# Performance work log

Hardware: AMD Instinct MI355X
Metric: run time of the kernel (lower is better)

## Reference

```python
import jax, jax.numpy as jnp
import numpy as np

B, T, E, H = 4, 1024, 1024, 16
F = E // H  # head_feature = 64
EPS = 1e-5


def setup_inputs() -> dict:
    key = jax.random.key(0)
    ks = jax.random.split(key, 7)
    return {
        "x": jax.random.normal(ks[0], (B, T, E), dtype=jnp.float32),
        "q_w": jax.random.normal(ks[1], (H, E, F), dtype=jnp.float32),
        "k_w": jax.random.normal(ks[2], (H, E, F), dtype=jnp.float32),
        "v_w": jax.random.normal(ks[3], (H, E, F), dtype=jnp.float32),
        "fr_w": jax.random.normal(ks[4], (B, E, E), dtype=jnp.float32),
        "ff_w": jax.random.normal(ks[5], (E, E), dtype=jnp.float32),
        "ff_b": jax.random.normal(ks[6], (E,), dtype=jnp.float32),
        "ln1_w": jnp.ones((T, E), dtype=jnp.float32),
        "ln1_b": jnp.zeros((T, E), dtype=jnp.float32),
        "ln2_w": jnp.ones((T, E), dtype=jnp.float32),
        "ln2_b": jnp.zeros((T, E), dtype=jnp.float32),
    }


def _layernorm_2d(x, w, b):
    # LayerNorm over the last TWO dims ([T, E]), matching nn.LayerNorm([T, E])
    mean = jnp.mean(x, axis=(-2, -1), keepdims=True)
    var = jnp.mean(jnp.square(x - mean), axis=(-2, -1), keepdims=True)
    return (x - mean) * jax.lax.rsqrt(var + EPS) * w + b


def _attention(x, q_w, k_w, v_w, fr_w):
    # projections: [B,T,E] x [H,E,F] -> [B,H,T,F]
    q = jnp.einsum("bte,hef->bhtf", x, q_w)
    k = jnp.einsum("bte,hef->bhtf", x, k_w)
    v = jnp.einsum("bte,hef->bhtf", x, v_w)
    scores = jnp.einsum("bhqf,bhkf->bhqk", q, k)  # [B,H,T,T]
    # faithful to source: multiplicative mask (-1e9 on strict upper tri, +1 added everywhere)
    ones = jnp.ones((T, T), dtype=scores.dtype)
    mask = -1.0e9 * jnp.triu(ones, k=1) + ones
    scores = scores * mask
    attn = jax.nn.softmax(scores / jnp.sqrt(jnp.float32(F)), axis=-1)
    z = jnp.einsum("bhqk,bhkf->bhqf", attn, v)  # [B,H,T,F]
    z = z.transpose(0, 2, 1, 3).reshape(B, T, E)  # merge heads
    return jnp.einsum("bte,bed->btd", z, fr_w)  # per-batch feature reduction


def reference(x, q_w, k_w, v_w, fr_w, ff_w, ff_b, ln1_w, ln1_b, ln2_w, ln2_b):
    z = _attention(x, q_w, k_w, v_w, fr_w)
    z1 = _layernorm_2d(x + z, ln1_w, ln1_b)
    z2 = jax.nn.relu(jnp.einsum("bte,de->btd", z1, ff_w) + ff_b)
    return _layernorm_2d(z1 + z2, ln2_w, ln2_b)
```

## Files before the change

kernel.cpp:

```cpp
#include <hip/hip_runtime.h>
#include <math.h>

constexpr int Bc = 4, Tc = 1024, Ec = 1024, Hc = 16, Fc = 64;

typedef __attribute__((ext_vector_type(8))) short bf16x8;
typedef __attribute__((ext_vector_type(4))) float f32x4;

__device__ __forceinline__ ushort f2bf(float x) {
  union { float f; unsigned u; } v; v.f = x;
  unsigned r = v.u + 0x7fffu + ((v.u >> 16) & 1u);
  return (ushort)(r >> 16);
}
__device__ __forceinline__ float bf2f(ushort h) {
  union { float f; unsigned u; } v; v.u = ((unsigned)h) << 16; return v.f;
}
__device__ __forceinline__ void split3(float x, ushort& h, ushort& m, ushort& l) {
  h = f2bf(x);
  float r1 = x - bf2f(h);
  m = f2bf(r1);
  float r2 = r1 - bf2f(m);
  l = f2bf(r2);
}
__device__ __forceinline__ void split2(float x, ushort& h, ushort& l) {
  h = f2bf(x);
  l = f2bf(x - bf2f(h));
}
__device__ __forceinline__ void split3t(float x, ushort& h, ushort& m, ushort& l) {
  union { float f; unsigned u; } v; v.f = x;
  h = (ushort)(v.u >> 16);
  union { float f; unsigned u; } hf; hf.u = v.u & 0xffff0000u;
  float r1 = x - hf.f;
  union { float f; unsigned u; } v1; v1.f = r1;
  m = (ushort)(v1.u >> 16);
  union { float f; unsigned u; } mf; mf.u = v1.u & 0xffff0000u;
  float r2 = r1 - mf.f;
  union { float f; unsigned u; } v2; v2.f = r2;
  l = (ushort)(v2.u >> 16);
}

#define FRAG_IDX(tile, quad, l) (((((tile) * 4) + (quad)) * 16 + (l)) * 8)

__global__ __launch_bounds__(256) void prep_all(
    const float* __restrict__ qw, const float* __restrict__ kw,
    const float* __restrict__ vw, ushort* __restrict__ wT,
    const float* __restrict__ x, ushort* __restrict__ xh,
    ushort* __restrict__ xm, ushort* __restrict__ xl)
{
  const int zi = blockIdx.z;
  const int tid = threadIdx.x;
  if (zi >= 3) {
    const int bid = (zi - 3) * 256 + blockIdx.y * 16 + blockIdx.x;
    const int i = bid * 256 + tid;
    const float4 a = ((const float4*)x)[i * 2];
    const float4 b = ((const float4*)x)[i * 2 + 1];
    const float xs[8] = {a.x, a.y, a.z, a.w, b.x, b.y, b.z, b.w};
    bf16x8 h, m, l;
#pragma unroll
    for (int j = 0; j < 8; ++j) {
      ushort hu, mu, lu;
      split3t(xs[j], hu, mu, lu);
      h[j] = (short)hu; m[j] = (short)mu; l[j] = (short)lu;
    }
    ((bf16x8*)xh)[i] = h;
    ((bf16x8*)xm)[i] = m;
    ((bf16x8*)xl)[i] = l;
    return;
  }
  const float* src = (zi == 0) ? qw : (zi == 1) ? kw : vw;
  ushort* dst = wT + (size_t)(zi * 3) * (1u << 20);
  const int ns = (zi == 2) ? 1 : 3;
  const int h = blockIdx.y, e0 = blockIdx.x * 64;
  __shared__ float T[64][68];
  {
    const int er = tid >> 4, fr = (tid & 15) * 4;
#pragma unroll
    for (int i = 0; i < 4; ++i) {
      const float4 v = *(const float4*)&src[((size_t)(h * 1024 + e0 + er + i * 16)) * 64 + fr];
      *(float4*)&T[er + i * 16][fr] = v;
    }
  }
  __syncthreads();
  const int f = tid >> 2, eo = (tid & 3) * 16;
  ushort hs[16], ms[16], ls[16];
#pragma unroll
  for (int j = 0; j < 16; ++j) split3(T[eo + j][f], hs[j], ms[j], ls[j]);
  const size_t nbase = (size_t)(h * 64 + f) * 1024 + e0 + eo;
  bf16x8 v0, v1;
#pragma unroll
  for (int j = 0; j < 8; ++j) { v0[j] = (short)hs[j]; v1[j] = (short)hs[j + 8]; }
  *(bf16x8*)&dst[nbase] = v0; *(bf16x8*)&dst[nbase + 8] = v1;
  if (ns == 3) {
#pragma unroll
    for (int j = 0; j < 8; ++j) { v0[j] = (short)ms[j]; v1[j] = (short)ms[j + 8]; }
    *(bf16x8*)&dst[(1u << 20) + nbase] = v0; *(bf16x8*)&dst[(1u << 20) + nbase + 8] = v1;
#pragma unroll
    for (int j = 0; j < 8; ++j) { v0[j] = (short)ls[j]; v1[j] = (short)ls[j + 8]; }
    *(bf16x8*)&dst[(2u << 20) + nbase] = v0; *(bf16x8*)&dst[(2u << 20) + nbase + 8] = v1;
  }
}

__global__ __launch_bounds__(256) void transp_frw(
    const float* __restrict__ frw, ushort* __restrict__ frT)
{
  const int bb = blockIdx.z;
  const int e0 = blockIdx.x * 64, d0 = blockIdx.y * 64;
  __shared__ float T[64][68];
  const int tid = threadIdx.x;
  {
    const int er = tid >> 4, dr = (tid & 15) * 4;
#pragma unroll
    for (int i = 0; i < 4; ++i) {
      const float4 v = *(const float4*)&frw[((size_t)bb * 1024 + e0 + er + i * 16) * 1024 + d0 + dr];
      *(float4*)&T[er + i * 16][dr] = v;
    }
  }
  __syncthreads();
  const int d = tid >> 2, eo = (tid & 3) * 16;
  ushort hs[16], ls[16];
#pragma unroll
  for (int j = 0; j < 16; ++j) split2(T[eo + j][d], hs[j], ls[j]);
  const size_t nbase = ((size_t)bb * 1024 + d0 + d) * 1024 + e0 + eo;
  bf16x8 v0, v1;
#pragma unroll
  for (int j = 0; j < 8; ++j) { v0[j] = (short)hs[j]; v1[j] = (short)hs[j + 8]; }
  *(bf16x8*)&frT[nbase] = v0; *(bf16x8*)&frT[nbase + 8] = v1;
#pragma unroll
  for (int j = 0; j < 8; ++j) { v0[j] = (short)ls[j]; v1[j] = (short)ls[j + 8]; }
  *(bf16x8*)&frT[(4u << 20) + nbase] = v0; *(bf16x8*)&frT[(4u << 20) + nbase + 8] = v1;
}

__global__ __launch_bounds__(256) void proj_all_ps(
    const ushort* __restrict__ xh, const ushort* __restrict__ xm,
    const ushort* __restrict__ xl, const ushort* __restrict__ wT,
    float* __restrict__ qf, ushort* __restrict__ kh,
    ushort* __restrict__ km, ushort* __restrict__ kl,
    ushort* __restrict__ vt)
{
  const int zi = blockIdx.z;
  const int m0 = blockIdx.x * 128, n0 = blockIdx.y * 128;
  __shared__ ushort As[3 * 4096];
  __shared__ ushort Bs[3 * 4096];
  const int tid = threadIdx.x;
  const int wave = tid >> 6, lane = tid & 63, l15 = lane & 15, quad = lane >> 4;
  const int wm = wave >> 1, wn = wave & 1;
  const int sr = tid >> 1, q0 = (tid & 1) * 2;
  const int wb0 = FRAG_IDX(sr >> 4, q0, sr & 15);
  const int wb1 = FRAG_IDX(sr >> 4, q0 + 1, sr & 15);
  f32x4 acc[4][4] = {};

  const size_t arow = (size_t)(m0 + sr) * 1024 + q0 * 8;
  const ushort* axh = xh + arow;
  const ushort* axm = xm + arow;
  const ushort* axl = xl + arow;

  if (zi < 2) {
    const ushort* wt = wT + (size_t)zi * 3 * (1u << 20);
    const ushort* bpb = wt + (size_t)(n0 + sr) * 1024 + q0 * 8;
    bf16x8 pah0 = *(const bf16x8*)(axh);
    bf16x8 pah1 = *(const bf16x8*)(axh + 8);
    bf16x8 pam0 = *(const bf16x8*)(axm);
    bf16x8 pam1 = *(const bf16x8*)(axm + 8);
    bf16x8 pal0 = *(const bf16x8*)(axl);
    bf16x8 pal1 = *(const bf16x8*)(axl + 8);
    bf16x8 pb0[3], pb1[3];
#pragma unroll
    for (int s = 0; s < 3; ++s) {
      const ushort* bp = bpb + ((size_t)s << 20);
      pb0[s] = *(const bf16x8*)(bp);
      pb1[s] = *(const bf16x8*)(bp + 8);
    }
    for (int k0 = 0; k0 < 1024; k0 += 32) {
      __syncthreads();
      {
        *(bf16x8*)&As[wb0] = pah0;        *(bf16x8*)&As[wb1] = pah1;
        *(bf16x8*)&As[4096 + wb0] = pam0; *(bf16x8*)&As[4096 + wb1] = pam1;
        *(bf16x8*)&As[8192 + wb0] = pal0; *(bf16x8*)&As[8192 + wb1] = pal1;
#pragma unroll
        for (int s = 0; s < 3; ++s) {
          *(bf16x8*)&Bs[s * 4096 + wb0] = pb0[s];
          *(bf16x8*)&Bs[s * 4096 + wb1] = pb1[s];
        }
      }
      __syncthreads();
      if (k0 < 992) {
        const int ko = k0 + 32;
        pah0 = *(const bf16x8*)(axh + ko);
        pah1 = *(const bf16x8*)(axh + ko + 8);
        pam0 = *(const bf16x8*)(axm + ko);
        pam1 = *(const bf16x8*)(axm + ko + 8);
        pal0 = *(const bf16x8*)(axl + ko);
        pal1 = *(const bf16x8*)(axl + ko + 8);
#pragma unroll
        for (int s = 0; s < 3; ++s) {
          const ushort* bp = bpb + ((size_t)s << 20) + ko;
          pb0[s] = *(const bf16x8*)(bp);
          pb1[s] = *(const bf16x8*)(bp + 8);
        }
      }
      bf16x8 af[4][3];
#pragma unroll
      for (int tm = 0; tm < 4; ++tm)
#pragma unroll
        for (int s = 0; s < 3; ++s)
          af[tm][s] = *(const bf16x8*)&As[s * 4096 + FRAG_IDX(wm * 4 + tm, quad, l15)];
#pragma unroll
      for (int tn = 0; tn < 4; ++tn) {
        const int bi = FRAG_IDX(wn * 4 + tn, quad, l15);
        bf16x8 b0 = *(const bf16x8*)&Bs[bi];
        bf16x8 b1 = *(const bf16x8*)&Bs[4096 + bi];
        bf16x8 b2 = *(const bf16x8*)&Bs[8192 + bi];
#pragma unroll
        for (int tm = 0; tm < 4; ++tm) {
          f32x4 a = acc[tm][tn];
          a = __builtin_amdgcn_mfma_f32_16x16x32_bf16(af[tm][0], b0, a, 0, 0, 0);
          a = __builtin_amdgcn_mfma_f32_16x16x32_bf16(af[tm][0], b1, a, 0, 0, 0);
          a = __builtin_amdgcn_mfma_f32_16x16x32_bf16(af[tm][1], b0, a, 0, 0, 0);
          a = __builtin_amdgcn_mfma_f32_16x16x32_bf16(af[tm][0], b2, a, 0, 0, 0);
          a = __builtin_amdgcn_mfma_f32_16x16x32_bf16(af[tm][1], b1, a, 0, 0, 0);
          a = __builtin_amdgcn_mfma_f32_16x16x32_bf16(af[tm][2], b0, a, 0, 0, 0);
          acc[tm][tn] = a;
        }
      }
    }
#pragma unroll
    for (int tm = 0; tm < 4; ++tm) {
#pragma unroll
      for (int tn = 0; tn < 4; ++tn) {
#pragma unroll
        for (int r = 0; r < 4; ++r) {
          int m = m0 + wm * 64 + tm * 16 + quad * 4 + r;
          int n = n0 + wn * 64 + tn * 16 + l15;
          int b = m >> 10, t = m & 1023, h = n >> 6, f = n & 63;
          size_t idx = (((size_t)(b * 16 + h)) * 1024 + t) * 64 + f;
          if (zi == 0) {
            qf[idx] = acc[tm][tn][r];
          } else {
            ushort hu, mu, lu;
            split3(acc[tm][tn][r], hu, mu, lu);
            kh[idx] = hu; km[idx] = mu; kl[idx] = lu;
          }
        }
      }
    }
  } else {
    const ushort* wt = wT + (size_t)6 * (1u << 20);
    const ushort* bpb = wt + (size_t)(n0 + sr) * 1024 + q0 * 8;
    bf16x8 pah0 = *(const bf16x8*)(axh);
    bf16x8 pah1 = *(const bf16x8*)(axh + 8);
    bf16x8 pb0 = *(const bf16x8*)(bpb);
    bf16x8 pb1 = *(const bf16x8*)(bpb + 8);
    for (int k0 = 0; k0 < 1024; k0 += 32) {
      __syncthreads();
      {
        *(bf16x8*)&As[wb0] = pah0; *(bf16x8*)&As[wb1] = pah1;
        *(bf16x8*)&Bs[wb0] = pb0;  *(bf16x8*)&Bs[wb1] = pb1;
      }
      __syncthreads();
      if (k0 < 992) {
        const int ko = k0 + 32;
        pah0 = *(const bf16x8*)(axh + ko);
        pah1 = *(const bf16x8*)(axh + ko + 8);
        pb0 = *(const bf16x8*)(bpb + ko);
        pb1 = *(const bf16x8*)(bpb + ko + 8);
      }
      bf16x8 af[4];
#pragma unroll
      for (int tm = 0; tm < 4; ++tm)
        af[tm] = *(const bf16x8*)&As[FRAG_IDX(wm * 4 + tm, quad, l15)];
#pragma unroll
      for (int tn = 0; tn < 4; ++tn) {
        bf16x8 b0 = *(const bf16x8*)&Bs[FRAG_IDX(wn * 4 + tn, quad, l15)];
#pragma unroll
        for (int tm = 0; tm < 4; ++tm)
          acc[tm][tn] = __builtin_amdgcn_mfma_f32_16x16x32_bf16(af[tm], b0, acc[tm][tn], 0, 0, 0);
      }
    }
#pragma unroll
    for (int tm = 0; tm < 4; ++tm) {
#pragma unroll
      for (int tn = 0; tn < 4; ++tn) {
#pragma unroll
        for (int r = 0; r < 4; ++r) {
          int m = m0 + wm * 64 + tm * 16 + quad * 4 + r;
          int n = n0 + wn * 64 + tn * 16 + l15;
          int b = m >> 10, t = m & 1023, h = n >> 6, f = n & 63;
          vt[(((size_t)(b * 16 + h)) * 64 + f) * 1024 + t] = f2bf(acc[tm][tn][r]);
        }
      }
    }
  }
}

__global__ __launch_bounds__(256) void proj_all_mfma(
    const float* __restrict__ x, const ushort* __restrict__ wT,
    float* __restrict__ qf, ushort* __restrict__ kh,
    ushort* __restrict__ km, ushort* __restrict__ kl,
    ushort* __restrict__ vt)
{
  const int zi = blockIdx.z;
  const int m0 = blockIdx.x * 128, n0 = blockIdx.y * 128;
  __shared__ ushort As[3 * 4096];
  __shared__ ushort Bs[3 * 4096];
  const int tid = threadIdx.x;
  const int wave = tid >> 6, lane = tid & 63, l15 = lane & 15, quad = lane >> 4;
  const int wm = wave >> 1, wn = wave & 1;
  const int sr = tid >> 1, q0 = (tid & 1) * 2;
  const int wb0 = FRAG_IDX(sr >> 4, q0, sr & 15);
  const int wb1 = FRAG_IDX(sr >> 4, q0 + 1, sr & 15);
  f32x4 acc[4][4] = {};

  const float* apx = x + (size_t)(m0 + sr) * 1024 + q0 * 8;
  float4 px0 = *(const float4*)(apx);
  float4 px1 = *(const float4*)(apx + 4);
  float4 px2 = *(const float4*)(apx + 8);
  float4 px3 = *(const float4*)(apx + 12);

  if (zi < 2) {
    const ushort* wt = wT + (size_t)zi * 3 * (1u << 20);
    const ushort* bpb = wt + (size_t)(n0 + sr) * 1024 + q0 * 8;
    bf16x8 pb0[3], pb1[3];
#pragma unroll
    for (int s = 0; s < 3; ++s) {
      const ushort* bp = bpb + ((size_t)s << 20);
      pb0[s] = *(const bf16x8*)(bp);
      pb1[s] = *(const bf16x8*)(bp + 8);
    }
    for (int k0 = 0; k0 < 1024; k0 += 32) {
      __syncthreads();
      {
        float xs[16];
        *(float4*)&xs[0]  = px0;
        *(float4*)&xs[4]  = px1;
        *(float4*)&xs[8]  = px2;
        *(float4*)&xs[12] = px3;
        bf16x8 h0, h1, m0v, m1v, l0, l1;
#pragma unroll
        for (int j = 0; j < 8; ++j) {
          ushort hu, mu, lu;
          split3t(xs[j], hu, mu, lu);
          h0[j] = (short)hu; m0v[j] = (short)mu; l0[j] = (short)lu;
          split3t(xs[j + 8], hu, mu, lu);
          h1[j] = (short)hu; m1v[j] = (short)mu; l1[j] = (short)lu;
        }
        *(bf16x8*)&As[wb0] = h0;          *(bf16x8*)&As[wb1] = h1;
        *(bf16x8*)&As[4096 + wb0] = m0v;  *(bf16x8*)&As[4096 + wb1] = m1v;
        *(bf16x8*)&As[8192 + wb0] = l0;   *(bf16x8*)&As[8192 + wb1] = l1;
#pragma unroll
        for (int s = 0; s < 3; ++s) {
          *(bf16x8*)&Bs[s * 4096 + wb0] = pb0[s];
          *(bf16x8*)&Bs[s * 4096 + wb1] = pb1[s];
        }
      }
      __syncthreads();
      if (k0 < 992) {
        const float* nx = apx + k0 + 32;
        px0 = *(const float4*)(nx);
        px1 = *(const float4*)(nx + 4);
        px2 = *(const float4*)(nx + 8);
        px3 = *(const float4*)(nx + 12);
#pragma unroll
        for (int s = 0; s < 3; ++s) {
          const ushort* bp = bpb + ((size_t)s << 20) + k0 + 32;
          pb0[s] = *(const bf16x8*)(bp);
          pb1[s] = *(const bf16x8*)(bp + 8);
        }
      }
      bf16x8 af[4][3];
#pragma unroll
      for (int tm = 0; tm < 4; ++tm)
#pragma unroll
        for (int s = 0; s < 3; ++s)
          af[tm][s] = *(const bf16x8*)&As[s * 4096 + FRAG_IDX(wm * 4 + tm, quad, l15)];
#pragma unroll
      for (int tn = 0; tn < 4; ++tn) {
        const int bi = FRAG_IDX(wn * 4 + tn, quad, l15);
        bf16x8 b0 = *(const bf16x8*)&Bs[bi];
        bf16x8 b1 = *(const bf16x8*)&Bs[4096 + bi];
        bf16x8 b2 = *(const bf16x8*)&Bs[8192 + bi];
#pragma unroll
        for (int tm = 0; tm < 4; ++tm) {
          f32x4 a = acc[tm][tn];
          a = __builtin_amdgcn_mfma_f32_16x16x32_bf16(af[tm][0], b0, a, 0, 0, 0);
          a = __builtin_amdgcn_mfma_f32_16x16x32_bf16(af[tm][0], b1, a, 0, 0, 0);
          a = __builtin_amdgcn_mfma_f32_16x16x32_bf16(af[tm][1], b0, a, 0, 0, 0);
          a = __builtin_amdgcn_mfma_f32_16x16x32_bf16(af[tm][0], b2, a, 0, 0, 0);
          a = __builtin_amdgcn_mfma_f32_16x16x32_bf16(af[tm][1], b1, a, 0, 0, 0);
          a = __builtin_amdgcn_mfma_f32_16x16x32_bf16(af[tm][2], b0, a, 0, 0, 0);
          acc[tm][tn] = a;
        }
      }
    }
#pragma unroll
    for (int tm = 0; tm < 4; ++tm) {
#pragma unroll
      for (int tn = 0; tn < 4; ++tn) {
#pragma unroll
        for (int r = 0; r < 4; ++r) {
          int m = m0 + wm * 64 + tm * 16 + quad * 4 + r;
          int n = n0 + wn * 64 + tn * 16 + l15;
          int b = m >> 10, t = m & 1023, h = n >> 6, f = n & 63;
          size_t idx = (((size_t)(b * 16 + h)) * 1024 + t) * 64 + f;
          if (zi == 0) {
            qf[idx] = acc[tm][tn][r];
          } else {
            ushort hu, mu, lu;
            split3(acc[tm][tn][r], hu, mu, lu);
            kh[idx] = hu; km[idx] = mu; kl[idx] = lu;
          }
        }
      }
    }
  } else {
    const ushort* wt = wT + (size_t)6 * (1u << 20);
    const ushort* bpb = wt + (size_t)(n0 + sr) * 1024 + q0 * 8;
    bf16x8 pb0 = *(const bf16x8*)(bpb);
    bf16x8 pb1 = *(const bf16x8*)(bpb + 8);
    for (int k0 = 0; k0 < 1024; k0 += 32) {
      __syncthreads();
      {
        float xs[16];
        *(float4*)&xs[0]  = px0;
        *(float4*)&xs[4]  = px1;
        *(float4*)&xs[8]  = px2;
        *(float4*)&xs[12] = px3;
        bf16x8 h0, h1;
#pragma unroll
        for (int j = 0; j < 8; ++j) {
          h0[j] = (short)f2bf(xs[j]);
          h1[j] = (short)f2bf(xs[j + 8]);
        }
        *(bf16x8*)&As[wb0] = h0; *(bf16x8*)&As[wb1] = h1;
        *(bf16x8*)&Bs[wb0] = pb0; *(bf16x8*)&Bs[wb1] = pb1;
      }
      __syncthreads();
      if (k0 < 992) {
        const float* nx = apx + k0 + 32;
        px0 = *(const float4*)(nx);
        px1 = *(const float4*)(nx + 4);
        px2 = *(const float4*)(nx + 8);
        px3 = *(const float4*)(nx + 12);
        pb0 = *(const bf16x8*)(bpb + k0 + 32);
        pb1 = *(const bf16x8*)(bpb + k0 + 40);
      }
      bf16x8 af[4];
#pragma unroll
      for (int tm = 0; tm < 4; ++tm)
        af[tm] = *(const bf16x8*)&As[FRAG_IDX(wm * 4 + tm, quad, l15)];
#pragma unroll
      for (int tn = 0; tn < 4; ++tn) {
        bf16x8 b0 = *(const bf16x8*)&Bs[FRAG_IDX(wn * 4 + tn, quad, l15)];
#pragma unroll
        for (int tm = 0; tm < 4; ++tm)
          acc[tm][tn] = __builtin_amdgcn_mfma_f32_16x16x32_bf16(af[tm], b0, acc[tm][tn], 0, 0, 0);
      }
    }
#pragma unroll
    for (int tm = 0; tm < 4; ++tm) {
#pragma unroll
      for (int tn = 0; tn < 4; ++tn) {
#pragma unroll
        for (int r = 0; r < 4; ++r) {
          int m = m0 + wm * 64 + tm * 16 + quad * 4 + r;
          int n = n0 + wn * 64 + tn * 16 + l15;
          int b = m >> 10, t = m & 1023, h = n >> 6, f = n & 63;
          vt[(((size_t)(b * 16 + h)) * 64 + f) * 1024 + t] = f2bf(acc[tm][tn][r]);
        }
      }
    }
  }
}

__global__ __launch_bounds__(512) void attn_mfma(
    const float* __restrict__ qf, const ushort* __restrict__ kh,
    const ushort* __restrict__ km, const ushort* __restrict__ kl,
    const ushort* __restrict__ vt, ushort* __restrict__ zh, ushort* __restrict__ zl)
{
  __shared__ ushort Ks[3][64][68];
  __shared__ ushort Vs[64][68];
  __shared__ ushort Pl[8][16][68];

  const int tid = threadIdx.x;
  const int wave = tid >> 6, lane = tid & 63;
  const int l15 = lane & 15, quad = lane >> 4;
  const int bh = blockIdx.y;
  const int qbase = blockIdx.x * 128;

  bf16x8 aqh[2], aqm[2], aql[2];
  {
    const int qrow = qbase + wave * 16 + l15;
    const float* qp = qf + ((size_t)bh * Tc + qrow) * Fc;
#pragma unroll
    for (int ks = 0; ks < 2; ++ks) {
      int f0 = ks * 32 + quad * 8;
      float4 x0 = *(const float4*)(qp + f0);
      float4 x1 = *(const float4*)(qp + f0 + 4);
      float xs[8] = {x0.x, x0.y, x0.z, x0.w, x1.x, x1.y, x1.z, x1.w};
#pragma unroll
      for (int j = 0; j < 8; ++j) {
        ushort hu, mu, lu;
        split3(xs[j], hu, mu, lu);
        aqh[ks][j] = (short)hu; aqm[ks][j] = (short)mu; aql[ks][j] = (short)lu;
      }
    }
  }

  f32x4 o[4] = {{0,0,0,0},{0,0,0,0},{0,0,0,0},{0,0,0,0}};
  float m_run[4], l_run[4];
#pragma unroll
  for (int r = 0; r < 4; ++r) { m_run[r] = -1e30f; l_run[r] = 0.f; }

  const int srow = tid >> 3, sc8 = tid & 7;
  const size_t kbase = (size_t)bh * Tc * Fc;
  const size_t vbase = (size_t)bh * Fc * Tc;
  const ushort* kp0 = kh + kbase + (size_t)srow * Fc + sc8 * 8;
  const ushort* kp1 = km + kbase + (size_t)srow * Fc + sc8 * 8;
  const ushort* kp2 = kl + kbase + (size_t)srow * Fc + sc8 * 8;
  const ushort* vp  = vt + vbase + (size_t)srow * Tc + sc8 * 8;

  for (int kt = 0; kt < Tc; kt += 64) {
    __syncthreads();
    {
      const size_t ko = (size_t)kt * Fc;
      *(bf16x8*)&Ks[0][srow][sc8 * 8] = *(const bf16x8*)(kp0 + ko);
      *(bf16x8*)&Ks[1][srow][sc8 * 8] = *(const bf16x8*)(kp1 + ko);
      *(bf16x8*)&Ks[2][srow][sc8 * 8] = *(const bf16x8*)(kp2 + ko);
      *(bf16x8*)&Vs[srow][sc8 * 8]    = *(const bf16x8*)(vp + kt);
    }
    __syncthreads();

    f32x4 sacc[4] = {{0,0,0,0},{0,0,0,0},{0,0,0,0},{0,0,0,0}};
#pragma unroll
    for (int nt = 0; nt < 4; ++nt) {
      int key = nt * 16 + l15;
#pragma unroll
      for (int ks = 0; ks < 2; ++ks) {
        int f0 = ks * 32 + quad * 8;
        bf16x8 bh_ = *(const bf16x8*)&Ks[0][key][f0];
        bf16x8 bm_ = *(const bf16x8*)&Ks[1][key][f0];
        bf16x8 bl_ = *(const bf16x8*)&Ks[2][key][f0];
        sacc[nt] = __builtin_amdgcn_mfma_f32_16x16x32_bf16(aqh[ks], bh_, sacc[nt], 0, 0, 0);
        sacc[nt] = __builtin_amdgcn_mfma_f32_16x16x32_bf16(aqh[ks], bm_, sacc[nt], 0, 0, 0);
        sacc[nt] = __builtin_amdgcn_mfma_f32_16x16x32_bf16(aqm[ks], bh_, sacc[nt], 0, 0, 0);
        sacc[nt] = __builtin_amdgcn_mfma_f32_16x16x32_bf16(aqh[ks], bl_, sacc[nt], 0, 0, 0);
        sacc[nt] = __builtin_amdgcn_mfma_f32_16x16x32_bf16(aqm[ks], bm_, sacc[nt], 0, 0, 0);
        sacc[nt] = __builtin_amdgcn_mfma_f32_16x16x32_bf16(aql[ks], bh_, sacc[nt], 0, 0, 0);
      }
    }

    const int rowg0 = qbase + wave * 16 + quad * 4;
    float mx[4];
#pragma unroll
    for (int r = 0; r < 4; ++r) mx[r] = -1e30f;
#pragma unroll
    for (int nt = 0; nt < 4; ++nt) {
      int key = kt + nt * 16 + l15;
#pragma unroll
      for (int r = 0; r < 4; ++r) {
        float s = sacc[nt][r];
        if (key > rowg0 + r) s *= -1.0e9f + 1.0f;
        s *= 0.125f;
        sacc[nt][r] = s;
        mx[r] = fmaxf(mx[r], s);
      }
    }
#pragma unroll
    for (int r = 0; r < 4; ++r)
#pragma unroll
      for (int d = 1; d < 16; d <<= 1) mx[r] = fmaxf(mx[r], __shfl_xor(mx[r], d));

    float corr[4], ps[4];
#pragma unroll
    for (int r = 0; r < 4; ++r) {
      float m2 = fmaxf(m_run[r], mx[r]);
      corr[r] = __expf(m_run[r] - m2);
      m_run[r] = m2;
      ps[r] = 0.f;
    }
#pragma unroll
    for (int nt = 0; nt < 4; ++nt) {
#pragma unroll
      for (int r = 0; r < 4; ++r) {
        float p = __expf(sacc[nt][r] - m_run[r]);
        ps[r] += p;
        Pl[wave][quad * 4 + r][nt * 16 + l15] = f2bf(p);
      }
    }
#pragma unroll
    for (int r = 0; r < 4; ++r) {
#pragma unroll
      for (int d = 1; d < 16; d <<= 1) ps[r] += __shfl_xor(ps[r], d);
      l_run[r] = l_run[r] * corr[r] + ps[r];
#pragma unroll
      for (int ft = 0; ft < 4; ++ft) o[ft][r] *= corr[r];
    }

#pragma unroll
    for (int ks2 = 0; ks2 < 2; ++ks2) {
      bf16x8 pa = *(const bf16x8*)&Pl[wave][l15][ks2 * 32 + quad * 8];
#pragma unroll
      for (int ft = 0; ft < 4; ++ft) {
        bf16x8 vb = *(const bf16x8*)&Vs[ft * 16 + l15][ks2 * 32 + quad * 8];
        o[ft] = __builtin_amdgcn_mfma_f32_16x16x32_bf16(pa, vb, o[ft], 0, 0, 0);
      }
    }
  }

  const int b = bh >> 4, h = bh & 15;
#pragma unroll
  for (int r = 0; r < 4; ++r) {
    float inv = 1.f / l_run[r];
    int row = qbase + wave * 16 + quad * 4 + r;
    size_t base = ((size_t)(b * Tc + row)) * Ec + h * Fc;
#pragma unroll
    for (int ft = 0; ft < 4; ++ft) {
      ushort hu, lu;
      split2(o[ft][r] * inv, hu, lu);
      zh[base + ft * 16 + l15] = hu;
      zl[base + ft * 16 + l15] = lu;
    }
  }
}

__global__ __launch_bounds__(256) void gemm_fr_mfma(
    const ushort* __restrict__ zh, const ushort* __restrict__ zl,
    const ushort* __restrict__ frT, const float* __restrict__ x,
    float* __restrict__ s1, float2* __restrict__ part)
{
  const int bb = blockIdx.z;
  const int m0 = blockIdx.x * 128, n0 = blockIdx.y * 64;
  __shared__ ushort Ah[4096], Al[4096], Bh[2048], Bl[2048];
  __shared__ float2 red[256];
  const int tid = threadIdx.x;
  const int wave = tid >> 6, lane = tid & 63, l15 = lane & 15, quad = lane >> 4;
  const int wm = wave >> 1, wn = wave & 1;
  const int sr = tid >> 1, q0 = (tid & 1) * 2;
  const int wb0 = FRAG_IDX(sr >> 4, q0, sr & 15);
  const int wb1 = FRAG_IDX(sr >> 4, q0 + 1, sr & 15);
  const int sr2 = tid >> 2, qb = tid & 3;
  const int wbB = FRAG_IDX(sr2 >> 4, qb, sr2 & 15);
  f32x4 acc[4][2] = {};
  const size_t abase = ((size_t)bb * 1024 + m0 + sr) * 1024 + q0 * 8;
  const size_t bbase = ((size_t)bb * 1024 + n0 + sr2) * 1024 + qb * 8;
  const ushort* blp = frT + (4u << 20);
  bf16x8 pAh0 = *(const bf16x8*)(zh + abase);
  bf16x8 pAh1 = *(const bf16x8*)(zh + abase + 8);
  bf16x8 pAl0 = *(const bf16x8*)(zl + abase);
  bf16x8 pAl1 = *(const bf16x8*)(zl + abase + 8);
  bf16x8 pBh  = *(const bf16x8*)(frT + bbase);
  bf16x8 pBl  = *(const bf16x8*)(blp + bbase);
  for (int k0 = 0; k0 < 1024; k0 += 32) {
    __syncthreads();
    {
      *(bf16x8*)&Ah[wb0] = pAh0;
      *(bf16x8*)&Ah[wb1] = pAh1;
      *(bf16x8*)&Al[wb0] = pAl0;
      *(bf16x8*)&Al[wb1] = pAl1;
      *(bf16x8*)&Bh[wbB] = pBh;
      *(bf16x8*)&Bl[wbB] = pBl;
    }
    __syncthreads();
    if (k0 < 992) {
      pAh0 = *(const bf16x8*)(zh + abase + k0 + 32);
      pAh1 = *(const bf16x8*)(zh + abase + k0 + 40);
      pAl0 = *(const bf16x8*)(zl + abase + k0 + 32);
      pAl1 = *(const bf16x8*)(zl + abase + k0 + 40);
      pBh  = *(const bf16x8*)(frT + bbase + k0 + 32);
      pBl  = *(const bf16x8*)(blp + bbase + k0 + 32);
    }
    bf16x8 ah[4], al[4];
#pragma unroll
    for (int tm = 0; tm < 4; ++tm) {
      ah[tm] = *(const bf16x8*)&Ah[FRAG_IDX(wm * 4 + tm, quad, l15)];
      al[tm] = *(const bf16x8*)&Al[FRAG_IDX(wm * 4 + tm, quad, l15)];
    }
#pragma unroll
    for (int tn = 0; tn < 2; ++tn) {
      const int bi = FRAG_IDX(wn * 2 + tn, quad, l15);
      bf16x8 b0 = *(const bf16x8*)&Bh[bi];
      bf16x8 b1 = *(const bf16x8*)&Bl[bi];
#pragma unroll
      for (int tm = 0; tm < 4; ++tm) {
        f32x4 a = acc[tm][tn];
        a = __builtin_amdgcn_mfma_f32_16x16x32_bf16(ah[tm], b0, a, 0, 0, 0);
        a = __builtin_amdgcn_mfma_f32_16x16x32_bf16(ah[tm], b1, a, 0, 0, 0);
        a = __builtin_amdgcn_mfma_f32_16x16x32_bf16(al[tm], b0, a, 0, 0, 0);
        acc[tm][tn] = a;
      }
    }
  }
  float sum = 0.f, sq = 0.f;
#pragma unroll
  for (int tm = 0; tm < 4; ++tm) {
#pragma unroll
    for (int tn = 0; tn < 2; ++tn) {
#pragma unroll
      for (int r = 0; r < 4; ++r) {
        int m = m0 + wm * 64 + tm * 16 + quad * 4 + r;
        int n = n0 + wn * 32 + tn * 16 + l15;
        size_t idx = ((size_t)bb * 1024 + m) * 1024 + n;
        float o = x[idx] + acc[tm][tn][r];
        s1[idx] = o;
        sum += o; sq += o * o;
      }
    }
  }
  red[tid] = make_float2(sum, sq);
  __syncthreads();
  for (int s = 128; s > 0; s >>= 1) {
    if (tid < s) { red[tid].x += red[tid + s].x; red[tid].y += red[tid + s].y; }
    __syncthreads();
  }
  if (tid == 0) part[bb * 128 + blockIdx.x * 16 + blockIdx.y] = red[0];
}

__global__ __launch_bounds__(256) void gemm_ff_mfma(
    const ushort* __restrict__ z1h, const ushort* __restrict__ z1l,
    const ushort* __restrict__ fwh, const ushort* __restrict__ fwl,
    const float* __restrict__ ffb, float* __restrict__ s2,
    float2* __restrict__ part)
{
  const int m0 = blockIdx.x * 128, n0 = blockIdx.y * 64;
  __shared__ ushort Ah[4096], Al[4096], Bh[2048], Bl[2048];
  __shared__ float2 red[256];
  const int tid = threadIdx.x;
  const int wave = tid >> 6, lane = tid & 63, l15 = lane & 15, quad = lane >> 4;
  const int wm = wave >> 1, wn = wave & 1;
  const int sr = tid >> 1, q0 = (tid & 1) * 2;
  const int wb0 = FRAG_IDX(sr >> 4, q0, sr & 15);
  const int wb1 = FRAG_IDX(sr >> 4, q0 + 1, sr & 15);
  const int sr2 = tid >> 2, qb = tid & 3;
  const int wbB = FRAG_IDX(sr2 >> 4, qb, sr2 & 15);
  f32x4 acc[4][2] = {};
  const size_t abase = (size_t)(m0 + sr) * 1024 + q0 * 8;
  const size_t bbase = (size_t)(n0 + sr2) * 1024 + qb * 8;
  bf16x8 pAh0 = *(const bf16x8*)(z1h + abase);
  bf16x8 pAh1 = *(const bf16x8*)(z1h + abase + 8);
  bf16x8 pAl0 = *(const bf16x8*)(z1l + abase);
  bf16x8 pAl1 = *(const bf16x8*)(z1l + abase + 8);
  bf16x8 pBh  = *(const bf16x8*)(fwh + bbase);
  bf16x8 pBl  = *(const bf16x8*)(fwl + bbase);
  for (int k0 = 0; k0 < 1024; k0 += 32) {
    __syncthreads();
    {
      *(bf16x8*)&Ah[wb0] = pAh0;
      *(bf16x8*)&Ah[wb1] = pAh1;
      *(bf16x8*)&Al[wb0] = pAl0;
      *(bf16x8*)&Al[wb1] = pAl1;
      *(bf16x8*)&Bh[wbB] = pBh;
      *(bf16x8*)&Bl[wbB] = pBl;
    }
    __syncthreads();
    if (k0 < 992) {
      pAh0 = *(const bf16x8*)(z1h + abase + k0 + 32);
      pAh1 = *(const bf16x8*)(z1h + abase + k0 + 40);
      pAl0 = *(const bf16x8*)(z1l + abase + k0 + 32);
      pAl1 = *(const bf16x8*)(z1l + abase + k0 + 40);
      pBh  = *(const bf16x8*)(fwh + bbase + k0 + 32);
      pBl  = *(const bf16x8*)(fwl + bbase + k0 + 32);
    }
    bf16x8 ah[4], al[4];
#pragma unroll
    for (int tm = 0; tm < 4; ++tm) {
      ah[tm] = *(const bf16x8*)&Ah[FRAG_IDX(wm * 4 + tm, quad, l15)];
      al[tm] = *(const bf16x8*)&Al[FRAG_IDX(wm * 4 + tm, quad, l15)];
    }
#pragma unroll
    for (int tn = 0; tn < 2; ++tn) {
      const int bi = FRAG_IDX(wn * 2 + tn, quad, l15);
      bf16x8 b0 = *(const bf16x8*)&Bh[bi];
      bf16x8 b1 = *(const bf16x8*)&Bl[bi];
#pragma unroll
      for (int tm = 0; tm < 4; ++tm) {
        f32x4 a = acc[tm][tn];
        a = __builtin_amdgcn_mfma_f32_16x16x32_bf16(ah[tm], b0, a, 0, 0, 0);
        a = __builtin_amdgcn_mfma_f32_16x16x32_bf16(ah[tm], b1, a, 0, 0, 0);
        a = __builtin_amdgcn_mfma_f32_16x16x32_bf16(al[tm], b0, a, 0, 0, 0);
        acc[tm][tn] = a;
      }
    }
  }
  float sum = 0.f, sq = 0.f;
#pragma unroll
  for (int tm = 0; tm < 4; ++tm) {
#pragma unroll
    for (int tn = 0; tn < 2; ++tn) {
#pragma unroll
      for (int r = 0; r < 4; ++r) {
        int m = m0 + wm * 64 + tm * 16 + quad * 4 + r;
        int n = n0 + wn * 32 + tn * 16 + l15;
        size_t idx = (size_t)m * 1024 + n;
        float z1v = bf2f(z1h[idx]) + bf2f(z1l[idx]);
        float o = z1v + fmaxf(acc[tm][tn][r] + ffb[n], 0.f);
        s2[idx] = o;
        sum += o; sq += o * o;
      }
    }
  }
  red[tid] = make_float2(sum, sq);
  __syncthreads();
  for (int s = 128; s > 0; s >>= 1) {
    if (tid < s) { red[tid].x += red[tid + s].x; red[tid].y += red[tid + s].y; }
    __syncthreads();
  }
  if (tid == 0) part[blockIdx.x * 16 + blockIdx.y] = red[0];
}

__global__ __launch_bounds__(256) void ln_stats(
    const float2* __restrict__ part, float2* __restrict__ stats, int npart)
{
  __shared__ double sd[256], sq[256];
  const int tid = threadIdx.x;
  double as = 0.0, aq = 0.0;
  for (int i = tid; i < npart; i += 256) {
    float2 p = part[blockIdx.x * npart + i];
    as += (double)p.x; aq += (double)p.y;
  }
  sd[tid] = as; sq[tid] = aq;
  __syncthreads();
  for (int s = 128; s > 0; s >>= 1) {
    if (tid < s) { sd[tid] += sd[tid + s]; sq[tid] += sq[tid + s]; }
    __syncthreads();
  }
  if (tid == 0) {
    const double n = (double)Tc * Ec;
    double mean = sd[0] / n;
    double var = sq[0] / n - mean * mean;
    if (var < 0.0) var = 0.0;
    double rs = 1.0 / sqrt(var + 1e-5);
    stats[blockIdx.x] = make_float2((float)mean, (float)rs);
  }
}

__global__ __launch_bounds__(256) void ln_norm_split(
    const float* __restrict__ s, const float2* __restrict__ stats,
    const float* __restrict__ w, const float* __restrict__ bias,
    ushort* __restrict__ oh, ushort* __restrict__ ol,
    const float* __restrict__ ffw, ushort* __restrict__ fwh, ushort* __restrict__ fwl)
{
  if (blockIdx.x >= 4096) {
    int i = (blockIdx.x - 4096) * 256 + threadIdx.x;
#pragma unroll
    for (int j = 0; j < 4; ++j) {
      int idx = i * 4 + j;
      float4 v = ((const float4*)ffw)[idx];
      ushort4 h, l;
      split2(v.x, h.x, l.x); split2(v.y, h.y, l.y);
      split2(v.z, h.z, l.z); split2(v.w, h.w, l.w);
      ((ushort4*)fwh)[idx] = h; ((ushort4*)fwl)[idx] = l;
    }
    return;
  }
  int i = blockIdx.x * 256 + threadIdx.x;
  int b = i >> 18;
  int te4 = i & ((1 << 18) - 1);
  float2 st = stats[b];
  float4 sv = ((const float4*)s)[i];
  float4 wv = ((const float4*)w)[te4];
  float4 bv = ((const float4*)bias)[te4];
  float4 o;
  o.x = (sv.x - st.x) * st.y * wv.x + bv.x;
  o.y = (sv.y - st.x) * st.y * wv.y + bv.y;
  o.z = (sv.z - st.x) * st.y * wv.z + bv.z;
  o.w = (sv.w - st.x) * st.y * wv.w + bv.w;
  ushort4 h, l;
  split2(o.x, h.x, l.x); split2(o.y, h.y, l.y);
  split2(o.z, h.z, l.z); split2(o.w, h.w, l.w);
  ((ushort4*)oh)[i] = h; ((ushort4*)ol)[i] = l;
}

__global__ __launch_bounds__(256) void ln_norm(
    const float* __restrict__ s, const float2* __restrict__ stats,
    const float* __restrict__ w, const float* __restrict__ bias,
    float* __restrict__ out)
{
  int i = blockIdx.x * 256 + threadIdx.x;
  if (i >= (Bc * Tc * Ec) / 4) return;
  int b = i >> 18;
  int te4 = i & ((1 << 18) - 1);
  float2 st = stats[b];
  float4 sv = ((const float4*)s)[i];
  float4 wv = ((const float4*)w)[te4];
  float4 bv = ((const float4*)bias)[te4];
  float4 o;
  o.x = (sv.x - st.x) * st.y * wv.x + bv.x;
  o.y = (sv.y - st.x) * st.y * wv.y + bv.y;
  o.z = (sv.z - st.x) * st.y * wv.z + bv.z;
  o.w = (sv.w - st.x) * st.y * wv.w + bv.w;
  ((float4*)out)[i] = o;
}

extern "C" void kernel_launch(void* const* d_in, const int* in_sizes, int n_in,
                              void* d_out, int out_size, void* d_ws, size_t ws_size,
                              hipStream_t stream)
{
  const float* x    = (const float*)d_in[0];
  const float* qw   = (const float*)d_in[1];
  const float* kw   = (const float*)d_in[2];
  const float* vw   = (const float*)d_in[3];
  const float* frw  = (const float*)d_in[4];
  const float* ffw  = (const float*)d_in[5];
  const float* ffb  = (const float*)d_in[6];
  const float* ln1w = (const float*)d_in[7];
  const float* ln1b = (const float*)d_in[8];
  const float* ln2w = (const float*)d_in[9];
  const float* ln2b = (const float*)d_in[10];
  float* out = (float*)d_out;
  char* W = (char*)d_ws;

  const size_t MB = 1ull << 20;
  float*  qf  = (float*)(W);
  ushort* kh  = (ushort*)(W + 16 * MB);
  ushort* km  = (ushort*)(W + 24 * MB);
  ushort* kl  = (ushort*)(W + 32 * MB);
  ushort* vt  = (ushort*)(W + 40 * MB);
  ushort* wT  = (ushort*)(W + 48 * MB);
  ushort* zh  = (ushort*)(W + 48 * MB);
  ushort* zl  = (ushort*)(W + 56 * MB);
  ushort* frT = (ushort*)(W + 16 * MB);
  float*  s1  = (float*)(W);
  ushort* z1h = (ushort*)(W + 16 * MB);
  ushort* z1l = (ushort*)(W + 24 * MB);
  ushort* fwh = (ushort*)(W + 48 * MB);
  ushort* fwl = (ushort*)(W + 50 * MB);
  float*  s2  = (float*)(W + 32 * MB);
  float2* part1  = (float2*)(W + 64 * MB);
  float2* part2  = part1 + 1024;
  float2* stats1 = part2 + 1024;
  float2* stats2 = stats1 + 4;
  ushort* xh = (ushort*)(W + 65 * MB);
  ushort* xm = (ushort*)(W + 73 * MB);
  ushort* xl = (ushort*)(W + 81 * MB);
  const bool big_ws = ws_size >= 90 * MB;

  if (big_ws) {
    prep_all<<<dim3(16, 16, 11), 256, 0, stream>>>(qw, kw, vw, wT, x, xh, xm, xl);
    proj_all_ps<<<dim3(32, 8, 3), 256, 0, stream>>>(xh, xm, xl, wT, qf, kh, km, kl, vt);
  } else {
    prep_all<<<dim3(16, 16, 3), 256, 0, stream>>>(qw, kw, vw, wT, x, xh, xm, xl);
    proj_all_mfma<<<dim3(32, 8, 3), 256, 0, stream>>>(x, wT, qf, kh, km, kl, vt);
  }
  attn_mfma<<<dim3(8, 64), 512, 0, stream>>>(qf, kh, km, kl, vt, zh, zl);
  transp_frw<<<dim3(16, 16, 4), 256, 0, stream>>>(frw, frT);
  gemm_fr_mfma<<<dim3(8, 16, 4), 256, 0, stream>>>(zh, zl, frT, x, s1, part1);
  ln_stats<<<dim3(4), 256, 0, stream>>>(part1, stats1, 128);
  ln_norm_split<<<dim3(4352), 256, 0, stream>>>(s1, stats1, ln1w, ln1b, z1h, z1l,
                                                ffw, fwh, fwl);
  gemm_ff_mfma<<<dim3(32, 16), 256, 0, stream>>>(z1h, z1l, fwh, fwl, ffb, s2, part2);
  ln_stats<<<dim3(4), 256, 0, stream>>>(part2, stats2, 128);
  ln_norm<<<dim3(4096), 256, 0, stream>>>(s2, stats2, ln2w, ln2b, out);
}
```

Before: 414.6 us.

## Prefetch attention K/V tiles into registers and fold LN stats into norm kernels

The attention loop now loads the next K/V tile into registers right after the shared-memory barrier, so global loads overlap with the MFMA work on the current tile. Separately, the two tiny ln_stats launches are removed: each normalization block reduces the 128 partials itself with wavefront shuffles in double precision. This cuts two kernel launches and their serialization gaps. In exchange, every norm block repeats a small redundant reduction and the attention loop holds more registers.

```diff
diff --git a/kernel.cpp b/kernel.cpp
--- a/kernel.cpp
+++ b/kernel.cpp
@@ -517,16 +517,27 @@
   const ushort* kp2 = kl + kbase + (size_t)srow * Fc + sc8 * 8;
   const ushort* vp  = vt + vbase + (size_t)srow * Tc + sc8 * 8;
 
+  bf16x8 pk0 = *(const bf16x8*)(kp0);
+  bf16x8 pk1 = *(const bf16x8*)(kp1);
+  bf16x8 pk2 = *(const bf16x8*)(kp2);
+  bf16x8 pv  = *(const bf16x8*)(vp);
+
   for (int kt = 0; kt < Tc; kt += 64) {
     __syncthreads();
     {
-      const size_t ko = (size_t)kt * Fc;
-      *(bf16x8*)&Ks[0][srow][sc8 * 8] = *(const bf16x8*)(kp0 + ko);
-      *(bf16x8*)&Ks[1][srow][sc8 * 8] = *(const bf16x8*)(kp1 + ko);
-      *(bf16x8*)&Ks[2][srow][sc8 * 8] = *(const bf16x8*)(kp2 + ko);
-      *(bf16x8*)&Vs[srow][sc8 * 8]    = *(const bf16x8*)(vp + kt);
+      *(bf16x8*)&Ks[0][srow][sc8 * 8] = pk0;
+      *(bf16x8*)&Ks[1][srow][sc8 * 8] = pk1;
+      *(bf16x8*)&Ks[2][srow][sc8 * 8] = pk2;
+      *(bf16x8*)&Vs[srow][sc8 * 8]    = pv;
     }
     __syncthreads();
+    if (kt < Tc - 64) {
+      const size_t ko = (size_t)(kt + 64) * Fc;
+      pk0 = *(const bf16x8*)(kp0 + ko);
+      pk1 = *(const bf16x8*)(kp1 + ko);
+      pk2 = *(const bf16x8*)(kp2 + ko);
+      pv  = *(const bf16x8*)(vp + kt + 64);
+    }
 
     f32x4 sacc[4] = {{0,0,0,0},{0,0,0,0},{0,0,0,0},{0,0,0,0}};
 #pragma unroll
@@ -805,34 +816,33 @@
   if (tid == 0) part[blockIdx.x * 16 + blockIdx.y] = red[0];
 }
 
-__global__ __launch_bounds__(256) void ln_stats(
-    const float2* __restrict__ part, float2* __restrict__ stats, int npart)
-{
-  __shared__ double sd[256], sq[256];
-  const int tid = threadIdx.x;
-  double as = 0.0, aq = 0.0;
-  for (int i = tid; i < npart; i += 256) {
-    float2 p = part[blockIdx.x * npart + i];
-    as += (double)p.x; aq += (double)p.y;
-  }
-  sd[tid] = as; sq[tid] = aq;
+__device__ __forceinline__ float2 ln_stats_inblock(
+    const float2* __restrict__ part, int b, int tid, float2* st_sh)
+{
+  if (tid < 64) {
+    float2 p0 = part[b * 128 + tid * 2];
+    float2 p1 = part[b * 128 + tid * 2 + 1];
+    double as = (double)p0.x + (double)p1.x;
+    double aq = (double)p0.y + (double)p1.y;
+#pragma unroll
+    for (int d = 1; d < 64; d <<= 1) {
+      as += __shfl_xor(as, d);
+      aq += __shfl_xor(aq, d);
+    }
+    if (tid == 0) {
+      const double n = (double)Tc * Ec;
+      double mean = as / n;
+      double var = aq / n - mean * mean;
+      if (var < 0.0) var = 0.0;
+      *st_sh = make_float2((float)mean, (float)(1.0 / sqrt(var + 1e-5)));
+    }
+  }
   __syncthreads();
-  for (int s = 128; s > 0; s >>= 1) {
-    if (tid < s) { sd[tid] += sd[tid + s]; sq[tid] += sq[tid + s]; }
-    __syncthreads();
-  }
-  if (tid == 0) {
-    const double n = (double)Tc * Ec;
-    double mean = sd[0] / n;
-    double var = sq[0] / n - mean * mean;
-    if (var < 0.0) var = 0.0;
-    double rs = 1.0 / sqrt(var + 1e-5);
-    stats[blockIdx.x] = make_float2((float)mean, (float)rs);
-  }
+  return *st_sh;
 }
 
 __global__ __launch_bounds__(256) void ln_norm_split(
-    const float* __restrict__ s, const float2* __restrict__ stats,
+    const float* __restrict__ s, const float2* __restrict__ part,
     const float* __restrict__ w, const float* __restrict__ bias,
     ushort* __restrict__ oh, ushort* __restrict__ ol,
     const float* __restrict__ ffw, ushort* __restrict__ fwh, ushort* __restrict__ fwl)
@@ -850,10 +860,12 @@
     }
     return;
   }
-  int i = blockIdx.x * 256 + threadIdx.x;
+  __shared__ float2 st_sh;
+  const int tid = threadIdx.x;
+  int i = blockIdx.x * 256 + tid;
   int b = i >> 18;
+  float2 st = ln_stats_inblock(part, b, tid, &st_sh);
   int te4 = i & ((1 << 18) - 1);
-  float2 st = stats[b];
   float4 sv = ((const float4*)s)[i];
   float4 wv = ((const float4*)w)[te4];
   float4 bv = ((const float4*)bias)[te4];
@@ -869,15 +881,16 @@
 }
 
 __global__ __launch_bounds__(256) void ln_norm(
-    const float* __restrict__ s, const float2* __restrict__ stats,
+    const float* __restrict__ s, const float2* __restrict__ part,
     const float* __restrict__ w, const float* __restrict__ bias,
     float* __restrict__ out)
 {
-  int i = blockIdx.x * 256 + threadIdx.x;
-  if (i >= (Bc * Tc * Ec) / 4) return;
+  __shared__ float2 st_sh;
+  const int tid = threadIdx.x;
+  int i = blockIdx.x * 256 + tid;
   int b = i >> 18;
+  float2 st = ln_stats_inblock(part, b, tid, &st_sh);
   int te4 = i & ((1 << 18) - 1);
-  float2 st = stats[b];
   float4 sv = ((const float4*)s)[i];
   float4 wv = ((const float4*)w)[te4];
   float4 bv = ((const float4*)bias)[te4];
@@ -925,8 +938,6 @@
   float*  s2  = (float*)(W + 32 * MB);
   float2* part1  = (float2*)(W + 64 * MB);
   float2* part2  = part1 + 1024;
-  float2* stats1 = part2 + 1024;
-  float2* stats2 = stats1 + 4;
   ushort* xh = (ushort*)(W + 65 * MB);
   ushort* xm = (ushort*)(W + 73 * MB);
   ushort* xl = (ushort*)(W + 81 * MB);
@@ -942,10 +953,8 @@
   attn_mfma<<<dim3(8, 64), 512, 0, stream>>>(qf, kh, km, kl, vt, zh, zl);
   transp_frw<<<dim3(16, 16, 4), 256, 0, stream>>>(frw, frT);
   gemm_fr_mfma<<<dim3(8, 16, 4), 256, 0, stream>>>(zh, zl, frT, x, s1, part1);
-  ln_stats<<<dim3(4), 256, 0, stream>>>(part1, stats1, 128);
-  ln_norm_split<<<dim3(4352), 256, 0, stream>>>(s1, stats1, ln1w, ln1b, z1h, z1l,
+  ln_norm_split<<<dim3(4352), 256, 0, stream>>>(s1, part1, ln1w, ln1b, z1h, z1l,
                                                 ffw, fwh, fwl);
   gemm_ff_mfma<<<dim3(32, 16), 256, 0, stream>>>(z1h, z1l, fwh, fwl, ffb, s2, part2);
-  ln_stats<<<dim3(4), 256, 0, stream>>>(part2, stats2, 128);
-  ln_norm<<<dim3(4096), 256, 0, stream>>>(s2, stats2, ln2w, ln2b, out);
-}
+  ln_norm<<<dim3(4096), 256, 0, stream>>>(s2, part2, ln2w, ln2b, out);
+}
```

New measurement: 403.4 us, median of 2. -2.7%, faster.
